# Optimization experiments

Hardware: AMD Instinct MI355X
Metric: run time of the kernel (lower is better)

Reference implementation:

```python
import jax, jax.numpy as jnp
import numpy as np

NUM_HEADS = 4
STEPS_PER_DAY = 288
NUM_LAYERS = 3


def _ln(x, g, b):
    mu = jnp.mean(x, -1, keepdims=True)
    var = jnp.mean((x - mu) ** 2, -1, keepdims=True)
    return (x - mu) * jax.lax.rsqrt(var + 1e-5) * g + b


def _mha(x, Wq, bq, Wk, bk, Wv, bv, Wo, bo):
    # x: (B, S, L, D); attention over L (the -2 dim), matching AttentionLayer
    B, S, L, D = x.shape
    hd = D // NUM_HEADS
    q = (x @ Wq + bq).reshape(B, S, L, NUM_HEADS, hd)
    k = (x @ Wk + bk).reshape(B, S, L, NUM_HEADS, hd)
    v = (x @ Wv + bv).reshape(B, S, L, NUM_HEADS, hd)
    s = jnp.einsum('bslhd,bsmhd->bshlm', q, k) * (hd ** -0.5)
    a = jax.nn.softmax(s, axis=-1)
    o = jnp.einsum('bshlm,bsmhd->bslhd', a, v).reshape(B, S, L, D)
    return o @ Wo + bo


def _sal(x, params, i, dim):
    # SelfAttentionLayer (eval mode: dropout = identity)
    Wq, bq, Wk, bk, Wv, bv, Wo, bo, W1, b1, W2, b2, g1, B1, g2, B2 = (p[i] for p in params)
    x = jnp.swapaxes(x, dim, -2)
    x = _ln(x + _mha(x, Wq, bq, Wk, bk, Wv, bv, Wo, bo), g1, B1)
    x = _ln(x + (jax.nn.relu(x @ W1 + b1) @ W2 + b2), g2, B2)
    return jnp.swapaxes(x, dim, -2)


def _forward(x, W_in, b_in, tod_emb, dow_emb, node_emb, adp_emb, tparams, sparams, Wout, bout):
    B, T, N, _ = x.shape
    tod_idx = jnp.clip((x[..., 1] * STEPS_PER_DAY).astype(jnp.int32), 0, STEPS_PER_DAY - 1)
    dow_idx = jnp.clip(x[..., 2].astype(jnp.int32), 0, 6)
    h = jnp.concatenate([
        x @ W_in + b_in,                                    # input_proj (B,T,N,24)
        tod_emb[tod_idx],                                   # (B,T,N,24)
        dow_emb[dow_idx],                                   # (B,T,N,24)
        jnp.broadcast_to(node_emb, (B, T, N, node_emb.shape[-1])),
        jnp.broadcast_to(adp_emb, (B,) + adp_emb.shape),    # (B,T,N,80)
    ], axis=-1)                                             # model_dim = 176
    for i in range(NUM_LAYERS):
        h = _sal(h, tparams, i, 1)   # temporal attention over in_steps
    for i in range(NUM_LAYERS):
        h = _sal(h, sparams, i, 2)   # spatial attention over nodes
    out = jnp.swapaxes(h, 1, 2).reshape(B, N, -1) @ Wout + bout  # (B,N,out_steps)
    return jnp.swapaxes(out.reshape(B, N, -1, 1), 1, 2)          # (B,out_steps,N,1)


def setup_inputs() -> dict:
    ks = iter(jax.random.split(jax.random.key(0), 80))
    B, T, N, D, L, FF = 32, 12, 307, 176, NUM_LAYERS, 256
    nrm = lambda *s: jax.random.normal(next(ks), s, jnp.float32) * 0.02
    x0 = jax.random.normal(next(ks), (B, T, N, 1), jnp.float32)   # traffic value
    tod = jax.random.uniform(next(ks), (B, T, N, 1), jnp.float32)  # tod fraction in [0,1)
    dow = jax.random.uniform(next(ks), (B, T, N, 1), jnp.float32) * 6.99  # dow in [0,7)
    inp = {'x': jnp.concatenate([x0, tod, dow], -1),
           'W_in': nrm(3, 24), 'b_in': nrm(24),
           'tod_emb': nrm(STEPS_PER_DAY, 24), 'dow_emb': nrm(7, 24),
           'node_emb': nrm(N, 24), 'adp_emb': nrm(T, N, 80),
           'Wout': nrm(T * D, 12), 'bout': nrm(12)}
    shapes = {'Wq': (L, D, D), 'bq': (L, D), 'Wk': (L, D, D), 'bk': (L, D),
              'Wv': (L, D, D), 'bv': (L, D), 'Wo': (L, D, D), 'bo': (L, D),
              'W1': (L, D, FF), 'b1': (L, FF), 'W2': (L, FF, D), 'b2': (L, D)}
    for pfx in ('t', 's'):
        for nm, sh in shapes.items():
            inp[pfx + nm] = nrm(*sh)
        inp[pfx + 'g1'] = jnp.ones((L, D)); inp[pfx + 'B1'] = jnp.zeros((L, D))
        inp[pfx + 'g2'] = jnp.ones((L, D)); inp[pfx + 'B2'] = jnp.zeros((L, D))
    return inp


def reference(x, W_in, b_in, tod_emb, dow_emb, node_emb, adp_emb,
              tWq, tbq, tWk, tbk, tWv, tbv, tWo, tbo, tW1, tb1, tW2, tb2, tg1, tB1, tg2, tB2,
              sWq, sbq, sWk, sbk, sWv, sbv, sWo, sbo, sW1, sb1, sW2, sb2, sg1, sB1, sg2, sB2,
              Wout, bout):
    tparams = (tWq, tbq, tWk, tbk, tWv, tbv, tWo, tbo, tW1, tb1, tW2, tb2, tg1, tB1, tg2, tB2)
    sparams = (sWq, sbq, sWk, sbk, sWv, sbv, sWo, sbo, sW1, sb1, sW2, sb2, sg1, sB1, sg2, sB2)
    return _forward(x, W_in, b_in, tod_emb, dow_emb, node_emb, adp_emb, tparams, sparams, Wout, bout)
```

## Files before the change

kernel.cpp:

```cpp
#include <hip/hip_runtime.h>

#define BB 32
#define TPB 3684L
#define TT 12
#define NN 307
#define DM 176
#define KP 192
#define FFD 256
#define NH 4
#define HD 44
#define NTILE 77
#define TS 584

typedef __bf16 bfv8 __attribute__((ext_vector_type(8)));
typedef float f32x4 __attribute__((ext_vector_type(4)));
typedef short sv4 __attribute__((ext_vector_type(4)));
typedef unsigned int uiv4 __attribute__((ext_vector_type(4)));
typedef unsigned long long ull;

__device__ __forceinline__ float b2f(unsigned short h) {
  return __uint_as_float(((unsigned)h) << 16);
}
__device__ __forceinline__ unsigned short f2b(float f) {
  unsigned u = __float_as_uint(f);
  return (unsigned short)((u + 0x7FFFu + ((u >> 16) & 1u)) >> 16);
}

__device__ __forceinline__ f32x4 mfma16x16x16bf(sv4 a, sv4 b, f32x4 c) {
#if __has_builtin(__builtin_amdgcn_mfma_f32_16x16x16bf16_1k)
  return __builtin_amdgcn_mfma_f32_16x16x16bf16_1k(a, b, c, 0, 0, 0);
#else
  f32x4 d = c;
  asm("v_mfma_f32_16x16x16_bf16 %0, %1, %2, %0\n\ts_nop 7\n\ts_nop 7"
      : "+v"(d) : "v"(a), "v"(b));
  return d;
#endif
}

__global__ void prep_weights(
    const float* __restrict__ tWq, const float* __restrict__ tWk,
    const float* __restrict__ tWv, const float* __restrict__ tWo,
    const float* __restrict__ tW1, const float* __restrict__ tW2,
    const float* __restrict__ sWq, const float* __restrict__ sWk,
    const float* __restrict__ sWv, const float* __restrict__ sWo,
    const float* __restrict__ sW1, const float* __restrict__ sW2,
    const float* __restrict__ tbq, const float* __restrict__ tbk,
    const float* __restrict__ tbv,
    const float* __restrict__ sbq, const float* __restrict__ sbk,
    const float* __restrict__ sbv,
    unsigned short* __restrict__ wbase, float* __restrict__ bqkv) {
  int layer = blockIdx.y;
  int mat = blockIdx.z;
  int li = layer % 3;
  bool tp = (layer < 3);
  unsigned short* dst = wbase + (long)layer * 229376;
  long idx = (long)blockIdx.x * 256 + threadIdx.x;
  if (mat == 0) {
    if (idx < 528 * 192) {
      int nn = idx / 192, k = idx % 192;
      float v = 0.f;
      if (k < 176) {
        int sel = nn / 176, c = nn % 176;
        const float* W = tp ? (sel == 0 ? tWq : sel == 1 ? tWk : tWv)
                            : (sel == 0 ? sWq : sel == 1 ? sWk : sWv);
        v = W[(long)li * 176 * 176 + k * 176 + c];
      }
      dst[idx] = f2b(v);
    }
    if (idx < 528) {
      int sel = idx / 176, c = idx % 176;
      const float* bb = tp ? (sel == 0 ? tbq : sel == 1 ? tbk : tbv)
                           : (sel == 0 ? sbq : sel == 1 ? sbk : sbv);
      bqkv[layer * 528 + idx] = bb[li * 176 + c];
    }
  } else if (mat == 1) {
    if (idx < 176 * 192) {
      int nn = idx / 192, k = idx % 192;
      int hh = k / 48, dd = k % 48;
      float v = (dd < 44)
          ? (tp ? tWo : sWo)[(long)li * 176 * 176 + (hh * 44 + dd) * 176 + nn]
          : 0.f;
      dst[101376 + idx] = f2b(v);
    }
  } else if (mat == 2) {
    if (idx < 256 * 192) {
      int nn = idx / 192, k = idx % 192;
      float v = (k < 176) ? (tp ? tW1 : sW1)[(long)li * 176 * 256 + k * 256 + nn] : 0.f;
      dst[135168 + idx] = f2b(v);
    }
  } else {
    if (idx < 176 * 256) {
      int nn = idx / 256, k = idx % 256;
      float v = (tp ? tW2 : sW2)[(long)li * 256 * 176 + k * 176 + nn];
      dst[184320 + idx] = f2b(v);
    }
  }
}

__global__ __launch_bounds__(256) void embed_kernel(
    const float* __restrict__ x, const float* __restrict__ W_in,
    const float* __restrict__ b_in, const float* __restrict__ tod,
    const float* __restrict__ dow, const float* __restrict__ node,
    const float* __restrict__ adp, float* __restrict__ h,
    unsigned short* __restrict__ hb, long tok0, long Mc) {
  long i = (long)blockIdx.x * 256 + threadIdx.x;
  if (i >= Mc * KP) return;
  int dp = (int)(i % KP);
  long tok = i / KP;
  if (dp >= DM) { hb[tok * KP + dp] = 0; return; }
  long tg = tok0 + tok;
  int n = (int)(tg % NN);
  long bt = tg / NN;
  int t = (int)(bt % TT);
  float v;
  int d = dp;
  if (d < 24) {
    const float* xp = x + tg * 3;
    v = xp[0] * W_in[d] + xp[1] * W_in[24 + d] + xp[2] * W_in[48 + d] + b_in[d];
  } else if (d < 48) {
    float x1 = x[tg * 3 + 1];
    int idx = (int)(x1 * 288.0f);
    idx = idx < 0 ? 0 : (idx > 287 ? 287 : idx);
    v = tod[idx * 24 + (d - 24)];
  } else if (d < 72) {
    float x2 = x[tg * 3 + 2];
    int idx = (int)x2;
    idx = idx < 0 ? 0 : (idx > 6 ? 6 : idx);
    v = dow[idx * 24 + (d - 48)];
  } else if (d < 96) {
    v = node[n * 24 + (d - 72)];
  } else {
    v = adp[((long)t * NN + n) * 80 + (d - 96)];
  }
  h[tok * DM + d] = v;
  hb[tok * KP + d] = f2b(v);
}

template <int KSTEPS, bool RELU, bool OUTBF16, bool QKVPAD>
__global__ __launch_bounds__(256) void gemm_bias(
    const unsigned short* __restrict__ A, int lda,
    const unsigned short* __restrict__ Wt, const float* __restrict__ bias,
    void* __restrict__ out, int ldo, long M, int N, int tpy, long PS) {
  int wave = threadIdx.x >> 6;
  int lane = threadIdx.x & 63;
  long wrow = ((long)blockIdx.x * 4 + wave) * 64;
  if (wrow >= M) return;
  int lrow = lane & 15;
  int kq = lane >> 4;
  bfv8 a[4][KSTEPS];
#pragma unroll
  for (int rf = 0; rf < 4; ++rf) {
    long ar = wrow + rf * 16 + lrow;
    if (ar >= M) ar = M - 1;
#pragma unroll
    for (int ks = 0; ks < KSTEPS; ++ks)
      a[rf][ks] = *(const bfv8*)(A + ar * (long)lda + kq * 8 + ks * 32);
  }
  int ntiles = N >> 4;
  int nt0 = blockIdx.y * tpy;
  int ntE = nt0 + tpy;
  if (ntE > ntiles) ntE = ntiles;
  for (int nt = nt0; nt < ntE; ++nt) {
    int col = nt * 16 + lrow;
    const unsigned short* bp = Wt + (long)col * lda + kq * 8;
    f32x4 acc[4] = {{0, 0, 0, 0}, {0, 0, 0, 0}, {0, 0, 0, 0}, {0, 0, 0, 0}};
#pragma unroll
    for (int ks = 0; ks < KSTEPS; ++ks) {
      bfv8 b = *(const bfv8*)(bp + ks * 32);
#pragma unroll
      for (int rf = 0; rf < 4; ++rf)
        acc[rf] = __builtin_amdgcn_mfma_f32_16x16x32_bf16(a[rf][ks], b, acc[rf], 0, 0, 0);
    }
    float bv = bias[col];
    long obase = 0;
    int ocol = col;
    if (QKVPAD) {
      int sel = col / 176, rem = col - sel * 176;
      int hh = rem / 44, dd = rem - hh * 44;
      obase = (long)(sel * 4 + hh) * PS;
      ocol = dd;
    }
#pragma unroll
    for (int rf = 0; rf < 4; ++rf) {
      long r0 = wrow + rf * 16 + kq * 4;
#pragma unroll
      for (int r = 0; r < 4; ++r) {
        if (r0 + r >= M) continue;
        float v = acc[rf][r] + bv;
        if (RELU) v = fmaxf(v, 0.f);
        long idx = QKVPAD ? (obase + (r0 + r) * 48 + ocol)
                          : ((r0 + r) * (long)ldo + ocol);
        if (OUTBF16)
          ((unsigned short*)out)[idx] = f2b(v);
        else
          ((float*)out)[idx] = v;
      }
    }
  }
  if (QKVPAD && blockIdx.y == 0) {
    long row = wrow + lane;
    if (row < M) {
#pragma unroll
      for (int p = 0; p < 12; ++p)
        *(ull*)((unsigned short*)out + (long)p * PS + row * 48 + 44) = 0ULL;
    }
  }
}

template <int KSTEPS, bool AHM>
__global__ __launch_bounds__(256) void gemm_ln_fused(
    const unsigned short* __restrict__ A, int lda,
    const unsigned short* __restrict__ Wt, const float* __restrict__ bias,
    const float* __restrict__ g, const float* __restrict__ beta,
    float* __restrict__ h, unsigned short* __restrict__ hb,
    long M, long PS) {
  __shared__ float2 part[64][5];
  int w = threadIdx.x >> 6;
  int lane = threadIdx.x & 63;
  long wrow = (long)blockIdx.x * 64;
  if (wrow >= M) return;
  int lrow = lane & 15;
  int kq = lane >> 4;
  bfv8 a[4][KSTEPS];
#pragma unroll
  for (int rf = 0; rf < 4; ++rf) {
    long ar = wrow + rf * 16 + lrow;
    if (ar >= M) ar = M - 1;
#pragma unroll
    for (int ks = 0; ks < KSTEPS; ++ks) {
      if (AHM) {
        int kp0 = ks * 32 + kq * 8;
        int hh = kp0 / 48;
        int off = kp0 - hh * 48;
        a[rf][ks] = *(const bfv8*)(A + (long)hh * PS + ar * 48 + off);
      } else {
        a[rf][ks] = *(const bfv8*)(A + ar * (long)lda + kq * 8 + ks * 32);
      }
    }
  }
  f32x4 acc[3][4];
#pragma unroll
  for (int i = 0; i < 3; ++i) {
    int nt = w + 4 * i;
    if (nt >= 11) continue;
    int col = nt * 16 + lrow;
    const unsigned short* bp = Wt + (long)col * lda + kq * 8;
    f32x4 c0 = {0, 0, 0, 0}, c1 = {0, 0, 0, 0}, c2 = {0, 0, 0, 0}, c3 = {0, 0, 0, 0};
#pragma unroll
    for (int ks = 0; ks < KSTEPS; ++ks) {
      bfv8 b = *(const bfv8*)(bp + ks * 32);
      c0 = __builtin_amdgcn_mfma_f32_16x16x32_bf16(a[0][ks], b, c0, 0, 0, 0);
      c1 = __builtin_amdgcn_mfma_f32_16x16x32_bf16(a[1][ks], b, c1, 0, 0, 0);
      c2 = __builtin_amdgcn_mfma_f32_16x16x32_bf16(a[2][ks], b, c2, 0, 0, 0);
      c3 = __builtin_amdgcn_mfma_f32_16x16x32_bf16(a[3][ks], b, c3, 0, 0, 0);
    }
    acc[i][0] = c0; acc[i][1] = c1; acc[i][2] = c2; acc[i][3] = c3;
  }
  float sum[16], ss[16];
#pragma unroll
  for (int j = 0; j < 16; ++j) { sum[j] = 0.f; ss[j] = 0.f; }
#pragma unroll
  for (int i = 0; i < 3; ++i) {
    int nt = w + 4 * i;
    if (nt >= 11) continue;
    int col = nt * 16 + lrow;
    float bv = bias[col];
#pragma unroll
    for (int rf = 0; rf < 4; ++rf)
#pragma unroll
      for (int r = 0; r < 4; ++r) {
        long row = wrow + rf * 16 + kq * 4 + r;
        long rr = row < M ? row : M - 1;
        float v = acc[i][rf][r] + bv + h[rr * DM + col];
        acc[i][rf][r] = v;
        sum[rf * 4 + r] += v;
        ss[rf * 4 + r] += v * v;
      }
  }
#pragma unroll
  for (int j = 0; j < 16; ++j) {
#pragma unroll
    for (int o = 1; o < 16; o <<= 1) {
      sum[j] += __shfl_xor(sum[j], o);
      ss[j] += __shfl_xor(ss[j], o);
    }
  }
  if (lrow == 0) {
#pragma unroll
    for (int rf = 0; rf < 4; ++rf)
#pragma unroll
      for (int r = 0; r < 4; ++r)
        part[rf * 16 + kq * 4 + r][w] = float2{sum[rf * 4 + r], ss[rf * 4 + r]};
  }
  __syncthreads();
  if (w == 0) {
    float s = 0.f, q = 0.f;
#pragma unroll
    for (int ww = 0; ww < 4; ++ww) {
      float2 p = part[lane][ww];
      s += p.x; q += p.y;
    }
    float mean = s * (1.f / 176.f);
    float var = q * (1.f / 176.f) - mean * mean;
    part[lane][4] = float2{mean, rsqrtf(var + 1e-5f)};
  }
  __syncthreads();
#pragma unroll
  for (int i = 0; i < 3; ++i) {
    int nt = w + 4 * i;
    if (nt >= 11) continue;
    int col = nt * 16 + lrow;
    float gv = g[col], bv2 = beta[col];
#pragma unroll
    for (int rf = 0; rf < 4; ++rf)
#pragma unroll
      for (int r = 0; r < 4; ++r) {
        int lr = rf * 16 + kq * 4 + r;
        long row = wrow + lr;
        if (row >= M) continue;
        float2 st = part[lr][4];
        float y = (acc[i][rf][r] - st.x) * st.y * gv + bv2;
        h[row * DM + col] = y;
        hb[row * KP + col] = f2b(y);
      }
  }
  if (w == 0) {
    long row = wrow + lane;
    if (row < M) {
      ull* zp = (ull*)(hb + row * KP + DM);
      zp[0] = 0ULL; zp[1] = 0ULL; zp[2] = 0ULL; zp[3] = 0ULL;
    }
  }
}

__global__ __launch_bounds__(256) void attn_temporal_lds(
    const unsigned short* __restrict__ qkvh, unsigned short* __restrict__ atth,
    long PS) {
  __shared__ unsigned short ld[4 * 12 * TS];
  int tile = blockIdx.x % NTILE;
  int b = blockIdx.x / NTILE;
  int n0 = tile * 4;
  for (int idx = threadIdx.x; idx < 3456; idx += 256) {
    int p = idx / 288;
    int rem = idx % 288;
    int t = rem / 24;
    int rem2 = rem % 24;
    int j = rem2 / 6, e = rem2 % 6;
    uiv4 v = {0, 0, 0, 0};
    int n = n0 + j;
    if (n < NN)
      v = *(const uiv4*)(qkvh + (long)p * PS + ((long)(b * TT + t) * NN + n) * 48 + e * 8);
    *(uiv4*)(&ld[(j * 12 + p) * TS + t * 48 + e * 8]) = v;
  }
  __syncthreads();
  int tid = threadIdx.x;
  if (tid >= 192) return;
  int j = tid / 48, hl = tid % 48;
  int hh = hl / 12, l = hl % 12;
  int n = n0 + j;
  if (n >= NN) return;
  const float scale = 0.15075567228888181f;
  float q[HD];
  const unsigned short* qp = &ld[(j * 12 + hh) * TS + l * 48];
#pragma unroll
  for (int d = 0; d < HD; ++d) q[d] = b2f(qp[d]) * scale;
  float s[TT];
  float mx = -1e30f;
#pragma unroll
  for (int m = 0; m < TT; ++m) {
    const unsigned short* kp = &ld[(j * 12 + 4 + hh) * TS + m * 48];
    float acc = 0.f;
#pragma unroll
    for (int d = 0; d < HD; ++d) acc += q[d] * b2f(kp[d]);
    s[m] = acc;
    mx = fmaxf(mx, acc);
  }
  float den = 0.f;
#pragma unroll
  for (int m = 0; m < TT; ++m) { s[m] = __expf(s[m] - mx); den += s[m]; }
  float inv = 1.f / den;
  float o[HD];
#pragma unroll
  for (int d = 0; d < HD; ++d) o[d] = 0.f;
#pragma unroll
  for (int m = 0; m < TT; ++m) {
    const unsigned short* vp = &ld[(j * 12 + 8 + hh) * TS + m * 48];
    float p = s[m] * inv;
#pragma unroll
    for (int d = 0; d < HD; ++d) o[d] += p * b2f(vp[d]);
  }
  unsigned short* op = atth + (long)hh * PS + ((long)(b * TT + l) * NN + n) * 48;
#pragma unroll
  for (int d = 0; d < HD; d += 2) {
    unsigned u = (unsigned)f2b(o[d]) | ((unsigned)f2b(o[d + 1]) << 16);
    *(unsigned*)(op + d) = u;
  }
  *(ull*)(op + 44) = 0ULL;
}

#define KLS 72
#define VTS 332
__global__ __launch_bounds__(512, 2) void attn_spatial_mfma(
    const unsigned short* __restrict__ qkvh, unsigned short* __restrict__ atth,
    long PS) {
  __shared__ unsigned short Kl[320 * KLS];
  __shared__ unsigned short Vt[48 * VTS];
  int h = blockIdx.x & 3;
  int bt = blockIdx.x >> 2;
  long tokbase = (long)bt * NN;
  const unsigned short* qbase = qkvh + (long)h * PS + tokbase * 48;
  const unsigned short* kbase = qkvh + (long)(4 + h) * PS + tokbase * 48;
  const unsigned short* vbase = qkvh + (long)(8 + h) * PS + tokbase * 48;
  int tid = threadIdx.x;

  for (int idx = tid; idx < 320 * 8; idx += 512) {
    int m = idx >> 3, c = idx & 7;
    uiv4 v = {0, 0, 0, 0};
    if (c < 6 && m < NN) v = *(const uiv4*)(kbase + (long)m * 48 + c * 8);
    *(uiv4*)(&Kl[m * KLS + c * 8]) = v;
  }
  for (int task = tid; task < 480; task += 512) {
    int m0 = (task / 6) * 4, c = task % 6;
    const unsigned short* vb = vbase + c * 8;
    uiv4 r0 = {0, 0, 0, 0}, r1 = {0, 0, 0, 0}, r2 = {0, 0, 0, 0}, r3 = {0, 0, 0, 0};
    if (m0 + 0 < NN) r0 = *(const uiv4*)(vb + (long)(m0 + 0) * 48);
    if (m0 + 1 < NN) r1 = *(const uiv4*)(vb + (long)(m0 + 1) * 48);
    if (m0 + 2 < NN) r2 = *(const uiv4*)(vb + (long)(m0 + 2) * 48);
    if (m0 + 3 < NN) r3 = *(const uiv4*)(vb + (long)(m0 + 3) * 48);
#pragma unroll
    for (int j = 0; j < 8; ++j) {
      int w32 = j >> 1, sh = (j & 1) * 16;
      ull o = (ull)((r0[w32] >> sh) & 0xFFFFu) |
              ((ull)((r1[w32] >> sh) & 0xFFFFu) << 16) |
              ((ull)((r2[w32] >> sh) & 0xFFFFu) << 32) |
              ((ull)((r3[w32] >> sh) & 0xFFFFu) << 48);
      *(ull*)(&Vt[(c * 8 + j) * VTS + m0]) = o;
    }
  }
  __syncthreads();

  int w = tid >> 6;
  int lane = tid & 63;
  int lrow = lane & 15;
  int kq = lane >> 4;
  const float kscale = 0.2174944602f;

#pragma unroll
  for (int qi = 0; qi < 3; ++qi) {
    int qt = qi * 8 + w;
    if (qt >= 20) break;
    int ql = qt * 16 + lrow;
    int qc = ql < NN ? ql : NN - 1;
    const unsigned short* qrow = qbase + (long)qc * 48;
    bfv8 qb8a = *(const bfv8*)(qrow + kq * 8);
    bfv8 qb8b = *(const bfv8*)(qrow + 32 + kq * 8);

    float m_run = -1e30f, den = 0.f;
    f32x4 o0 = {0.f, 0.f, 0.f, 0.f}, o1 = {0.f, 0.f, 0.f, 0.f}, o2 = {0.f, 0.f, 0.f, 0.f};
#pragma unroll
    for (int ct = 0; ct < 20; ++ct) {
      const unsigned short* kp = &Kl[(ct * 16 + lrow) * KLS];
      bfv8 k8a = *(const bfv8*)(kp + kq * 8);
      bfv8 k8b = *(const bfv8*)(kp + 32 + kq * 8);
      f32x4 s = {0.f, 0.f, 0.f, 0.f};
      s = __builtin_amdgcn_mfma_f32_16x16x32_bf16(k8a, qb8a, s, 0, 0, 0);
      s = __builtin_amdgcn_mfma_f32_16x16x32_bf16(k8b, qb8b, s, 0, 0, 0);
#pragma unroll
      for (int r = 0; r < 4; ++r) {
        float v = s[r] * kscale;
        if (ct == 19 && (kq * 4 + r) >= 3) v = -1e30f;
        s[r] = v;
      }
      float smax = fmaxf(fmaxf(s[0], s[1]), fmaxf(s[2], s[3]));
      if (!__all(smax <= m_run + 8.f)) {
        smax = fmaxf(smax, __shfl_xor(smax, 16));
        smax = fmaxf(smax, __shfl_xor(smax, 32));
        float m_new = fmaxf(m_run, smax);
        float corr = exp2f(m_run - m_new);
        m_run = m_new;
        den *= corr;
        o0 = o0 * corr;
        o1 = o1 * corr;
        o2 = o2 * corr;
      }
      float p0 = exp2f(s[0] - m_run);
      float p1 = exp2f(s[1] - m_run);
      float p2 = exp2f(s[2] - m_run);
      float p3 = exp2f(s[3] - m_run);
      den += (p0 + p1) + (p2 + p3);
      sv4 pb = {(short)f2b(p0), (short)f2b(p1), (short)f2b(p2), (short)f2b(p3)};
      int mb = ct * 16 + kq * 4;
      sv4 a0 = *(const sv4*)(&Vt[(0 * 16 + lrow) * VTS + mb]);
      sv4 a1 = *(const sv4*)(&Vt[(1 * 16 + lrow) * VTS + mb]);
      sv4 a2 = *(const sv4*)(&Vt[(2 * 16 + lrow) * VTS + mb]);
      o0 = mfma16x16x16bf(a0, pb, o0);
      o1 = mfma16x16x16bf(a1, pb, o1);
      o2 = mfma16x16x16bf(a2, pb, o2);
    }
    den += __shfl_xor(den, 16);
    den += __shfl_xor(den, 32);
    float inv = 1.f / den;

    if (ql < NN) {
      unsigned short* dst = atth + (long)h * PS + (tokbase + ql) * 48;
      int db = kq * 4;
      {
        ull u = (ull)f2b(o0[0] * inv) | ((ull)f2b(o0[1] * inv) << 16) |
                ((ull)f2b(o0[2] * inv) << 32) | ((ull)f2b(o0[3] * inv) << 48);
        *(ull*)(dst + db) = u;
      }
      {
        ull u = (ull)f2b(o1[0] * inv) | ((ull)f2b(o1[1] * inv) << 16) |
                ((ull)f2b(o1[2] * inv) << 32) | ((ull)f2b(o1[3] * inv) << 48);
        *(ull*)(dst + 16 + db) = u;
      }
      if (db < 12) {
        ull u = (ull)f2b(o2[0] * inv) | ((ull)f2b(o2[1] * inv) << 16) |
                ((ull)f2b(o2[2] * inv) << 32) | ((ull)f2b(o2[3] * inv) << 48);
        *(ull*)(dst + 32 + db) = u;
      } else {
        *(ull*)(dst + 44) = 0ULL;
      }
    }
  }
}

__global__ __launch_bounds__(64) void out_kernel(
    const float* __restrict__ h, const float* __restrict__ Wout,
    const float* __restrict__ bout, float* __restrict__ out, int b0) {
  int bn = blockIdx.x;
  int n = bn % NN, bl = bn / NN;
  int b = b0 + bl;
  int lane = threadIdx.x;
  float acc[TT];
#pragma unroll
  for (int j = 0; j < TT; ++j) acc[j] = 0.f;
  for (int k = lane; k < TT * DM; k += 64) {
    int t = k / DM, d = k % DM;
    float a = h[((long)(bl * TT + t) * NN + n) * DM + d];
    const float* wp = Wout + (long)k * TT;
#pragma unroll
    for (int j = 0; j < TT; ++j) acc[j] += a * wp[j];
  }
#pragma unroll
  for (int j = 0; j < TT; ++j)
    for (int o = 32; o > 0; o >>= 1) acc[j] += __shfl_xor(acc[j], o);
  if (lane < TT) out[((long)b * TT + lane) * NN + n] = acc[lane] + bout[lane];
}

extern "C" void kernel_launch(void* const* d_in, const int* in_sizes, int n_in,
                              void* d_out, int out_size, void* d_ws, size_t ws_size,
                              hipStream_t stream) {
  char* ws = (char*)d_ws;
  unsigned short* wbase = (unsigned short*)ws;
  float* bqkv = (float*)(ws + 2752512L);
  char* dyn = ws + 2765184L;

  const long per_tok = 2624;
  int nb = 0;
  for (int c = 32; c >= 1; --c) {
    if (2765184L + (long)c * TPB * per_tok <= (long)ws_size) { nb = c; break; }
  }
  if (nb == 0) return;

  const long Mal = (long)nb * TPB;
  const long PS = Mal * 48;
  float* h = (float*)dyn;
  unsigned short* hb = (unsigned short*)(dyn + Mal * 704);
  unsigned short* qkvh = (unsigned short*)(dyn + Mal * 1088);
  unsigned short* mid = qkvh;
  unsigned short* atth = (unsigned short*)(dyn + Mal * 2240);

#define DF(i) ((const float*)d_in[i])

  prep_weights<<<dim3(396, 6, 4), 256, 0, stream>>>(
      DF(9), DF(11), DF(13), DF(15), DF(17), DF(19),
      DF(25), DF(27), DF(29), DF(31), DF(33), DF(35),
      DF(10), DF(12), DF(14), DF(26), DF(28), DF(30), wbase, bqkv);

  for (int b0 = 0; b0 < BB; b0 += nb) {
    int nb_cur = (BB - b0 < nb) ? (BB - b0) : nb;
    const long Mc = (long)nb_cur * TPB;
    int gx = (int)((Mc + 255) / 256);
    int gx64 = (int)((Mc + 63) / 64);

    embed_kernel<<<(int)((Mc * KP + 255) / 256), 256, 0, stream>>>(
        DF(0), DF(1), DF(2), DF(3), DF(4), DF(5), DF(6), h, hb,
        (long)b0 * TPB, Mc);

    for (int l = 0; l < 6; ++l) {
      int base = (l < 3) ? 9 : 25;
      int li = l % 3;
      const unsigned short* wl = wbase + (long)l * 229376;
      const unsigned short* Wqkv = wl;
      const unsigned short* Wo = wl + 101376;
      const unsigned short* W1 = wl + 135168;
      const unsigned short* W2 = wl + 184320;
      const float* bo = DF(base + 7) + li * 176;
      const float* b1 = DF(base + 9) + li * 256;
      const float* b2 = DF(base + 11) + li * 176;
      const float* g1 = DF(base + 12) + li * 176;
      const float* B1 = DF(base + 13) + li * 176;
      const float* g2 = DF(base + 14) + li * 176;
      const float* B2 = DF(base + 15) + li * 176;

      gemm_bias<6, false, true, true><<<dim3(gx, 3), 256, 0, stream>>>(
          hb, KP, Wqkv, bqkv + l * 528, qkvh, 0, Mc, 528, 11, PS);

      if (l < 3) {
        attn_temporal_lds<<<nb_cur * NTILE, 256, 0, stream>>>(qkvh, atth, PS);
      } else {
        attn_spatial_mfma<<<nb_cur * TT * NH, 512, 0, stream>>>(qkvh, atth, PS);
      }

      gemm_ln_fused<6, true><<<gx64, 256, 0, stream>>>(
          atth, KP, Wo, bo, g1, B1, h, hb, Mc, PS);

      gemm_bias<6, true, true, false><<<dim3(gx, 2), 256, 0, stream>>>(
          hb, KP, W1, b1, mid, FFD, Mc, FFD, 8, 0);

      gemm_ln_fused<8, false><<<gx64, 256, 0, stream>>>(
          mid, FFD, W2, b2, g2, B2, h, hb, Mc, 0);
    }

    out_kernel<<<nb_cur * NN, 64, 0, stream>>>(h, DF(7), DF(8), (float*)d_out, b0);
  }
#undef DF
}
```

Measured before the change: 3.673 ms.

## Fuse FFN up-projection, ReLU, down-projection and LayerNorm into one kernel

Replaces the separate W1 GEMM+ReLU kernel and the W2 GEMM+residual+LayerNorm kernel with a single kernel. Each 64-row block keeps its ReLU intermediate in shared memory (bf16), so the 256-wide mid activation no longer round-trips through global memory and one launch per layer is removed. In exchange, the larger LDS footprint may lower occupancy, and each block recomputes against the full weight matrices with less parallelism across output tiles.

Measured after the change: 3.134 ms, median of 2. 14.7% less time.

```diff
diff --git a/kernel.cpp b/kernel.cpp
--- a/kernel.cpp
+++ b/kernel.cpp
@@ -11,6 +11,7 @@
 #define HD 44
 #define NTILE 77
 #define TS 584
+#define MLS 264
 
 typedef __bf16 bfv8 __attribute__((ext_vector_type(8)));
 typedef float f32x4 __attribute__((ext_vector_type(4)));
@@ -333,6 +334,164 @@
   }
 }
 
+__global__ __launch_bounds__(256) void ffn_fused(
+    const unsigned short* __restrict__ A,
+    const unsigned short* __restrict__ W1t, const float* __restrict__ b1,
+    const unsigned short* __restrict__ W2t, const float* __restrict__ b2,
+    const float* __restrict__ g, const float* __restrict__ beta,
+    float* __restrict__ h, unsigned short* __restrict__ hb, long M) {
+  __shared__ unsigned short mid[64 * MLS];
+  __shared__ float2 part[64][5];
+  int w = threadIdx.x >> 6;
+  int lane = threadIdx.x & 63;
+  long wrow = (long)blockIdx.x * 64;
+  if (wrow >= M) return;
+  int lrow = lane & 15;
+  int kq = lane >> 4;
+  {
+    bfv8 a1[4][6];
+#pragma unroll
+    for (int rf = 0; rf < 4; ++rf) {
+      long ar = wrow + rf * 16 + lrow;
+      if (ar >= M) ar = M - 1;
+#pragma unroll
+      for (int ks = 0; ks < 6; ++ks)
+        a1[rf][ks] = *(const bfv8*)(A + ar * (long)KP + kq * 8 + ks * 32);
+    }
+#pragma unroll
+    for (int i = 0; i < 4; ++i) {
+      int nt = w * 4 + i;
+      int col = nt * 16 + lrow;
+      const unsigned short* bp = W1t + (long)col * KP + kq * 8;
+      f32x4 c0 = {0, 0, 0, 0}, c1 = {0, 0, 0, 0}, c2 = {0, 0, 0, 0}, c3 = {0, 0, 0, 0};
+#pragma unroll
+      for (int ks = 0; ks < 6; ++ks) {
+        bfv8 b = *(const bfv8*)(bp + ks * 32);
+        c0 = __builtin_amdgcn_mfma_f32_16x16x32_bf16(a1[0][ks], b, c0, 0, 0, 0);
+        c1 = __builtin_amdgcn_mfma_f32_16x16x32_bf16(a1[1][ks], b, c1, 0, 0, 0);
+        c2 = __builtin_amdgcn_mfma_f32_16x16x32_bf16(a1[2][ks], b, c2, 0, 0, 0);
+        c3 = __builtin_amdgcn_mfma_f32_16x16x32_bf16(a1[3][ks], b, c3, 0, 0, 0);
+      }
+      float bv = b1[col];
+      f32x4 cc[4] = {c0, c1, c2, c3};
+#pragma unroll
+      for (int rf = 0; rf < 4; ++rf)
+#pragma unroll
+        for (int r = 0; r < 4; ++r) {
+          float v = fmaxf(cc[rf][r] + bv, 0.f);
+          mid[(rf * 16 + kq * 4 + r) * MLS + col] = f2b(v);
+        }
+    }
+  }
+  __syncthreads();
+  f32x4 acc[3][4];
+#pragma unroll
+  for (int i = 0; i < 3; ++i)
+#pragma unroll
+    for (int rf = 0; rf < 4; ++rf) acc[i][rf] = f32x4{0.f, 0.f, 0.f, 0.f};
+#pragma unroll
+  for (int half = 0; half < 2; ++half) {
+    bfv8 a2[4][4];
+#pragma unroll
+    for (int rf = 0; rf < 4; ++rf)
+#pragma unroll
+      for (int ks = 0; ks < 4; ++ks)
+        a2[rf][ks] = *(const bfv8*)(&mid[(rf * 16 + lrow) * MLS + kq * 8 + (half * 4 + ks) * 32]);
+#pragma unroll
+    for (int i = 0; i < 3; ++i) {
+      int nt = w + 4 * i;
+      if (nt >= 11) continue;
+      int col = nt * 16 + lrow;
+      const unsigned short* bp = W2t + (long)col * FFD + kq * 8 + half * 128;
+      f32x4 c0 = acc[i][0], c1 = acc[i][1], c2 = acc[i][2], c3 = acc[i][3];
+#pragma unroll
+      for (int ks = 0; ks < 4; ++ks) {
+        bfv8 b = *(const bfv8*)(bp + ks * 32);
+        c0 = __builtin_amdgcn_mfma_f32_16x16x32_bf16(a2[0][ks], b, c0, 0, 0, 0);
+        c1 = __builtin_amdgcn_mfma_f32_16x16x32_bf16(a2[1][ks], b, c1, 0, 0, 0);
+        c2 = __builtin_amdgcn_mfma_f32_16x16x32_bf16(a2[2][ks], b, c2, 0, 0, 0);
+        c3 = __builtin_amdgcn_mfma_f32_16x16x32_bf16(a2[3][ks], b, c3, 0, 0, 0);
+      }
+      acc[i][0] = c0; acc[i][1] = c1; acc[i][2] = c2; acc[i][3] = c3;
+    }
+  }
+  float sum[16], ss[16];
+#pragma unroll
+  for (int j = 0; j < 16; ++j) { sum[j] = 0.f; ss[j] = 0.f; }
+#pragma unroll
+  for (int i = 0; i < 3; ++i) {
+    int nt = w + 4 * i;
+    if (nt >= 11) continue;
+    int col = nt * 16 + lrow;
+    float bv = b2[col];
+#pragma unroll
+    for (int rf = 0; rf < 4; ++rf)
+#pragma unroll
+      for (int r = 0; r < 4; ++r) {
+        long row = wrow + rf * 16 + kq * 4 + r;
+        long rr = row < M ? row : M - 1;
+        float v = acc[i][rf][r] + bv + h[rr * DM + col];
+        acc[i][rf][r] = v;
+        sum[rf * 4 + r] += v;
+        ss[rf * 4 + r] += v * v;
+      }
+  }
+#pragma unroll
+  for (int j = 0; j < 16; ++j) {
+#pragma unroll
+    for (int o = 1; o < 16; o <<= 1) {
+      sum[j] += __shfl_xor(sum[j], o);
+      ss[j] += __shfl_xor(ss[j], o);
+    }
+  }
+  if (lrow == 0) {
+#pragma unroll
+    for (int rf = 0; rf < 4; ++rf)
+#pragma unroll
+      for (int r = 0; r < 4; ++r)
+        part[rf * 16 + kq * 4 + r][w] = float2{sum[rf * 4 + r], ss[rf * 4 + r]};
+  }
+  __syncthreads();
+  if (w == 0) {
+    float s = 0.f, q = 0.f;
+#pragma unroll
+    for (int ww = 0; ww < 4; ++ww) {
+      float2 p = part[lane][ww];
+      s += p.x; q += p.y;
+    }
+    float mean = s * (1.f / 176.f);
+    float var = q * (1.f / 176.f) - mean * mean;
+    part[lane][4] = float2{mean, rsqrtf(var + 1e-5f)};
+  }
+  __syncthreads();
+#pragma unroll
+  for (int i = 0; i < 3; ++i) {
+    int nt = w + 4 * i;
+    if (nt >= 11) continue;
+    int col = nt * 16 + lrow;
+    float gv = g[col], bv2 = beta[col];
+#pragma unroll
+    for (int rf = 0; rf < 4; ++rf)
+#pragma unroll
+      for (int r = 0; r < 4; ++r) {
+        int lr = rf * 16 + kq * 4 + r;
+        long row = wrow + lr;
+        if (row >= M) continue;
+        float2 st = part[lr][4];
+        float y = (acc[i][rf][r] - st.x) * st.y * gv + bv2;
+        h[row * DM + col] = y;
+        hb[row * KP + col] = f2b(y);
+      }
+  }
+  if (w == 0) {
+    long row = wrow + lane;
+    if (row < M) {
+      ull* zp = (ull*)(hb + row * KP + DM);
+      zp[0] = 0ULL; zp[1] = 0ULL; zp[2] = 0ULL; zp[3] = 0ULL;
+    }
+  }
+}
+
 __global__ __launch_bounds__(256) void attn_temporal_lds(
     const unsigned short* __restrict__ qkvh, unsigned short* __restrict__ atth,
     long PS) {
@@ -568,7 +727,6 @@
   float* h = (float*)dyn;
   unsigned short* hb = (unsigned short*)(dyn + Mal * 704);
   unsigned short* qkvh = (unsigned short*)(dyn + Mal * 1088);
-  unsigned short* mid = qkvh;
   unsigned short* atth = (unsigned short*)(dyn + Mal * 2240);
 
 #define DF(i) ((const float*)d_in[i])
@@ -616,11 +774,8 @@
       gemm_ln_fused<6, true><<<gx64, 256, 0, stream>>>(
           atth, KP, Wo, bo, g1, B1, h, hb, Mc, PS);
 
-      gemm_bias<6, true, true, false><<<dim3(gx, 2), 256, 0, stream>>>(
-          hb, KP, W1, b1, mid, FFD, Mc, FFD, 8, 0);
-
-      gemm_ln_fused<8, false><<<gx64, 256, 0, stream>>>(
-          mid, FFD, W2, b2, g2, B2, h, hb, Mc, 0);
+      ffn_fused<<<gx64, 256, 0, stream>>>(
+          hb, W1, b1, W2, b2, g2, B2, h, hb, Mc);
     }
 
     out_kernel<<<nb_cur * NN, 64, 0, stream>>>(h, DF(7), DF(8), (float*)d_out, b0);
```
